# Performance work log

Hardware: AMD Instinct MI355X
Metric: run time of the kernel (lower is better)

Reference implementation:

```python
import jax, jax.numpy as jnp
import numpy as np

D_MODEL = 1024
NUM_HEADS = 16
D_K = D_MODEL // NUM_HEADS
ROPE_THETA = 10000.0


def _rope(x, positions):
    # x: [B, H, S, Dk]; positions: [S] int. Interleaved-pair RoPE, theta=10000.
    half = D_K // 2
    inv_freq = 1.0 / (ROPE_THETA ** (jnp.arange(half, dtype=jnp.float32) * 2.0 / D_K))
    ang = positions.astype(jnp.float32)[:, None] * inv_freq[None, :]  # [S, half]
    cos = jnp.cos(ang)[None, None]  # [1,1,S,half]
    sin = jnp.sin(ang)[None, None]
    x_even = x[..., 0::2]
    x_odd = x[..., 1::2]
    r_even = x_even * cos - x_odd * sin
    r_odd = x_even * sin + x_odd * cos
    out = jnp.stack([r_even, r_odd], axis=-1)  # [B,H,S,half,2]
    return out.reshape(x.shape)


def setup_inputs() -> dict:
    key = jax.random.key(0)
    ks = jax.random.split(key, 5)
    B, S = 4, 2048
    std = (2.0 / (D_MODEL + D_MODEL)) ** 0.5
    return {
        "x": jax.random.normal(ks[0], (B, S, D_MODEL), dtype=jnp.float32),
        "Wq": jax.random.normal(ks[1], (D_MODEL, D_MODEL), dtype=jnp.float32) * std,
        "Wk": jax.random.normal(ks[2], (D_MODEL, D_MODEL), dtype=jnp.float32) * std,
        "Wv": jax.random.normal(ks[3], (D_MODEL, D_MODEL), dtype=jnp.float32) * std,
        "Wo": jax.random.normal(ks[4], (D_MODEL, D_MODEL), dtype=jnp.float32) * std,
        "token_positions": jnp.arange(S, dtype=jnp.int32),
    }


def reference(x, Wq, Wk, Wv, Wo, token_positions):
    B, S, _ = x.shape
    # QKV projections (weights stored [out, in], y = x @ W^T)
    def proj(W):
        y = jnp.einsum('bsi,oi->bso', x, W)
        return y.reshape(B, S, NUM_HEADS, D_K).transpose(0, 2, 1, 3)  # [B,H,S,Dk]
    q = _rope(proj(Wq), token_positions)
    k = _rope(proj(Wk), token_positions)
    v = proj(Wv)
    scores = jnp.einsum('bhqd,bhkd->bhqk', q, k) / jnp.sqrt(jnp.float32(D_K))
    causal = token_positions[:, None] >= token_positions[None, :]  # [S,S]
    scores = jnp.where(causal[None, None], scores, jnp.float32(-1e9))
    probs = jax.nn.softmax(scores, axis=-1)
    attn = jnp.einsum('bhqk,bhkd->bhqd', probs, v)
    attn = attn.transpose(0, 2, 1, 3).reshape(B, S, D_MODEL)
    return jnp.einsum('bsi,oi->bso', attn, Wo)
```

## Files before the change

kernel.cpp:

```cpp
#include <hip/hip_runtime.h>
#include <hip/hip_bf16.h>
#include <math.h>

#define SEQ 2048
#define BATCH 4
#define MROWS (BATCH*SEQ)
#define DMODEL 1024
#define NHEADS 16
#define DKH 64

typedef float f32x4 __attribute__((ext_vector_type(4)));
typedef float f32x16 __attribute__((ext_vector_type(16)));
typedef __bf16 bf16x8 __attribute__((ext_vector_type(8)));
typedef unsigned short u16;
typedef unsigned int u32;
typedef u16 u16x4 __attribute__((ext_vector_type(4)));
typedef u16 u16x8 __attribute__((ext_vector_type(8)));
typedef u32 u32x4v __attribute__((ext_vector_type(4)));

__device__ __forceinline__ u16 f2bf(float f) {
  union { float f; unsigned u; } v; v.f = f;
  unsigned r = v.u + 0x7FFFu + ((v.u >> 16) & 1u);
  return (u16)(r >> 16);
}

__device__ __forceinline__ void async_copy16(const void* g, void* l) {
  __builtin_amdgcn_global_load_lds(
      (const __attribute__((address_space(1))) void*)g,
      (__attribute__((address_space(3))) void*)l, 16, 0, 0);
}

__device__ __forceinline__ u32 cvtpk(float lo, float hi) {
  u32 r;
  asm("v_cvt_pk_bf16_f32 %0, %1, %2" : "=v"(r) : "v"(lo), "v"(hi));
  return r;
}

__global__ __launch_bounds__(256) void k_prep(
    const float* __restrict__ x,
    const float* __restrict__ Wq, const float* __restrict__ Wk,
    const float* __restrict__ Wv, const float* __restrict__ Wo,
    const int* __restrict__ pos,
    u16* __restrict__ xb, u16* __restrict__ Wqb, u16* __restrict__ Wkb,
    u16* __restrict__ Wvb, u16* __restrict__ Wob,
    float* __restrict__ cosT, float* __restrict__ sinT)
{
  const int bid = blockIdx.x, tid = threadIdx.x;
  if (bid < 8192) {
    int i = bid*256 + tid;
    float4 v = ((const float4*)x)[i];
    u16x4 o; o[0]=f2bf(v.x); o[1]=f2bf(v.y); o[2]=f2bf(v.z); o[3]=f2bf(v.w);
    ((u16x4*)xb)[i] = o;
  } else if (bid < 12288) {
    int wi = (bid - 8192) >> 10;
    const float* src = (wi==0)?Wq:(wi==1)?Wk:(wi==2)?Wv:Wo;
    u16* dst = (wi==0)?Wqb:(wi==1)?Wkb:(wi==2)?Wvb:Wob;
    int i = ((bid - 8192) & 1023)*256 + tid;
    float4 v = ((const float4*)src)[i];
    u16x4 o; o[0]=f2bf(v.x); o[1]=f2bf(v.y); o[2]=f2bf(v.z); o[3]=f2bf(v.w);
    ((u16x4*)dst)[i] = o;
  } else {
    int i = (bid - 12288)*256 + tid;
    int s = i >> 5, j = i & 31;
    double p = (double)pos[s];
    double inv = pow(10000.0, -(double)j / 32.0);
    double a = p * inv;
    cosT[i] = (float)cos(a);
    sinT[i] = (float)sin(a);
  }
}

template<int MODE>
__global__ __launch_bounds__(512) void k_gemm2(
    const u16* __restrict__ A,
    const u16* __restrict__ W0, const u16* __restrict__ W1,
    const u16* __restrict__ W2,
    u16* __restrict__ Qo, u16* __restrict__ Ko, u16* __restrict__ Vto,
    float* __restrict__ Fo,
    const float* __restrict__ cosT, const float* __restrict__ sinT)
{
  __shared__ alignas(16) u16 As[3][128*64];
  __shared__ alignas(16) u16 Bs[3][256*64];

  const int B = blockIdx.x;
  const int bm = ((B & 7) << 3) | ((B >> 3) & 7);
  const int y  = B >> 6;
  int proj, bnl;
  const u16* W;
  if constexpr (MODE == 0) {
    proj = y >> 2; bnl = y & 3;
    W = (proj == 0) ? W0 : (proj == 1) ? W1 : W2;
  } else {
    proj = 3; bnl = y; W = W0;
  }

  const int tid = threadIdx.x;
  const int wave = tid >> 6, lane = tid & 63;
  const int lg = lane >> 4, lr = lane & 15;
  const int wm = wave >> 2, wn = wave & 3;

  const u16* Ab = A + (size_t)(bm*128)*DMODEL;
  const u16* Wb = W + (size_t)(bnl*256)*DMODEL;

  f32x4 acc[4][4];
#pragma unroll
  for (int i = 0; i < 4; ++i)
#pragma unroll
    for (int j = 0; j < 4; ++j) acc[i][j] = (f32x4){0,0,0,0};

  auto stage = [&](int buf, int kt) {
    const int k0 = kt * 64;
#pragma unroll
    for (int i = 0; i < 2; ++i) {
      const int idx = i*512 + tid;
      const int row = idx >> 3, ch = idx & 7;
      async_copy16(Ab + (size_t)row*DMODEL + k0 + ((ch ^ (row & 7)) * 8),
                   (char*)As[buf] + idx*16);
    }
#pragma unroll
    for (int i = 0; i < 4; ++i) {
      const int idx = i*512 + tid;
      const int row = idx >> 3, ch = idx & 7;
      async_copy16(Wb + (size_t)row*DMODEL + k0 + ((ch ^ (row & 7)) * 8),
                   (char*)Bs[buf] + idx*16);
    }
  };

  const int NT = DMODEL / 64;
  stage(0, 0);
  stage(1, 1);
  asm volatile("s_waitcnt vmcnt(6)" ::: "memory");
  __builtin_amdgcn_sched_barrier(0);
  __builtin_amdgcn_s_barrier();

  for (int t = 0; t < NT; ++t) {
    const int cur = t % 3;
    if (t + 2 < NT) stage((t + 2) % 3, t + 2);

    const u16* Aw = As[cur];
    const u16* Bw = Bs[cur];
    __builtin_amdgcn_s_setprio(1);
#pragma unroll
    for (int kk = 0; kk < 2; ++kk) {
      bf16x8 bfr[4];
#pragma unroll
      for (int ni = 0; ni < 4; ++ni) {
        const int row = wn*64 + ni*16 + lr;
        bfr[ni] = *(const bf16x8*)&Bw[row*64 + (((kk*4 + lg) ^ (row & 7)) * 8)];
      }
#pragma unroll
      for (int mi = 0; mi < 4; ++mi) {
        const int row = wm*64 + mi*16 + lr;
        bf16x8 af = *(const bf16x8*)&Aw[row*64 + (((kk*4 + lg) ^ (row & 7)) * 8)];
#pragma unroll
        for (int ni = 0; ni < 4; ++ni)
          acc[mi][ni] = __builtin_amdgcn_mfma_f32_16x16x32_bf16(af, bfr[ni], acc[mi][ni], 0, 0, 0);
      }
    }
    __builtin_amdgcn_s_setprio(0);

    if (t + 1 < NT) {
      if (t + 2 < NT) {
        asm volatile("s_waitcnt vmcnt(6)" ::: "memory");
      } else {
        asm volatile("s_waitcnt vmcnt(0)" ::: "memory");
      }
      __builtin_amdgcn_sched_barrier(0);
      __builtin_amdgcn_s_barrier();
    }
  }

#pragma unroll
  for (int mi = 0; mi < 4; ++mi) {
    const int row0 = bm*128 + wm*64 + mi*16 + lg*4;
#pragma unroll
    for (int ni = 0; ni < 4; ++ni) {
      const int col = bnl*256 + wn*64 + ni*16 + lr;
      f32x4 a = acc[mi][ni];
      if constexpr (MODE == 1) {
#pragma unroll
        for (int r = 0; r < 4; ++r) Fo[(size_t)(row0+r)*DMODEL + col] = a[r];
      } else {
        if (proj == 2) {
          const int hh = col >> 6, dd = col & 63;
          const int s0r = row0 & (SEQ-1);
          const int bb = row0 >> 11;
          u16x4 wv;
#pragma unroll
          for (int r = 0; r < 4; ++r) wv[r] = f2bf(a[r]);
          *(u16x4*)&Vto[((size_t)((bb*16+hh)*64 + dd))*SEQ + s0r] = wv;
        } else {
          u16* C = (proj == 0) ? Qo : Ko;
          const float scl = (proj == 0) ? 0.18033688f : 1.0f;
          const int dd = col & 63;
          const int j = dd >> 1;
          const float sgn = (dd & 1) ? 1.0f : -1.0f;
#pragma unroll
          for (int r = 0; r < 4; ++r) {
            const int s = (row0 + r) & (SEQ-1);
            float v = a[r];
            float pv = __shfl_xor(v, 1, 64);
            float c = cosT[s*32 + j], sn = sinT[s*32 + j];
            C[(size_t)(row0+r)*DMODEL + col] = f2bf((v*c + sgn*pv*sn) * scl);
          }
        }
      }
    }
  }
}

__global__ __launch_bounds__(512) void k_attn(
    const u16* __restrict__ Q, const u16* __restrict__ K,
    const u16* __restrict__ Vt, u16* __restrict__ O)
{
  const int B = blockIdx.x;
  const int bh = ((B & 7) << 3) | ((B >> 3) & 7);
  const int qt = 7 - (B >> 6);
  const int b = bh >> 4, h = bh & 15;
  const int wave = threadIdx.x >> 6, lane = threadIdx.x & 63;
  const int ql = lane & 31, hi = lane >> 5, hi4 = hi * 4;
  const int R0 = qt*256 + wave*32;

  __shared__ alignas(16) u16 Ks[2][64*64];
  __shared__ alignas(16) u16 Vs[2][64*64];

  const u16* Qb = Q + (size_t)(b*SEQ)*DMODEL + h*64;
  const u16* Kb = K + (size_t)(b*SEQ)*DMODEL + h*64;
  const u16* Vb = Vt + (size_t)(bh*64)*SEQ;

  bf16x8 qf[4];
#pragma unroll
  for (int j = 0; j < 4; ++j)
    qf[j] = *(const bf16x8*)(Qb + (size_t)(R0 + ql)*DMODEL + j*16 + hi*8);

  union { u16x8 u; bf16x8 v; } onesu;
#pragma unroll
  for (int i = 0; i < 8; ++i) onesu.u[i] = 0x3F80;
  const bf16x8 ones = onesu.v;

  f32x16 o0 = (f32x16)(0.f), o1 = (f32x16)(0.f);
  f32x16 lacc = (f32x16)(0.f);
  float m_run = -INFINITY;
  const float THR2 = 11.5415603f;

  const int KT = (qt + 1) * 4;

  const int qp = (ql & ~12) | ((ql & 4) << 1) | ((ql & 8) >> 1);

  auto stage = [&](int buf, int kt) {
    const int idx = threadIdx.x;
    const int row = idx >> 3, ch = idx & 7;
    const int sch = (ch ^ (row & 7)) * 8;
    const int k0 = kt * 64;
    async_copy16(Kb + (size_t)(k0 + row)*DMODEL + sch, (char*)Ks[buf] + idx*16);
    async_copy16(Vb + (size_t)row*SEQ + k0 + sch,      (char*)Vs[buf] + idx*16);
  };

  stage(0, 0);
  __syncthreads();

  for (int kt = 0; kt < KT; ++kt) {
    const int cur = kt & 1;
    if (kt + 1 < KT) stage(cur ^ 1, kt + 1);

    const int k0 = kt*64;
    if (k0 <= R0 + 31) {
      const u16* Kw = Ks[cur];
      const u16* Vw = Vs[cur];

      bf16x8 ka[2][4];
#pragma unroll
      for (int st = 0; st < 2; ++st)
#pragma unroll
        for (int j = 0; j < 4; ++j) {
          const int rk = st*32 + qp;
          const int c = (2*j + hi) ^ (rk & 7);
          ka[st][j] = *(const bf16x8*)&Kw[rk*64 + c*8];
        }
      f32x16 s0 = (f32x16)(0.f), s1 = (f32x16)(0.f);
#pragma unroll
      for (int j = 0; j < 4; ++j) {
        s0 = __builtin_amdgcn_mfma_f32_32x32x16_bf16(ka[0][j], qf[j], s0, 0, 0, 0);
        s1 = __builtin_amdgcn_mfma_f32_32x32x16_bf16(ka[1][j], qf[j], s1, 0, 0, 0);
      }

      if (k0 + 63 > R0) {
        const int base = k0 - R0;
#pragma unroll
        for (int r = 0; r < 16; ++r) {
          const int kl = (r & 7) + (hi << 3) + ((r & 8) << 1);
          s0[r] = (ql >= base + kl)      ? s0[r] : -1e30f;
          s1[r] = (ql >= base + 32 + kl) ? s1[r] : -1e30f;
        }
      }

      float t[16];
#pragma unroll
      for (int r = 0; r < 16; ++r) t[r] = fmaxf(s0[r], s1[r]);
#pragma unroll
      for (int w = 8; w >= 1; w >>= 1)
#pragma unroll
        for (int r = 0; r < w; ++r) t[r] = fmaxf(t[r], t[r+w]);
      const float mx = fmaxf(t[0], __shfl_xor(t[0], 32, 64));

      if (__any(mx > m_run + THR2)) {
        const float mn = fmaxf(m_run, mx);
        const float al = __builtin_exp2f(m_run - mn);
        m_run = mn;
        lacc[0] *= al;
#pragma unroll
        for (int r = 0; r < 16; ++r) { o0[r] *= al; o1[r] *= al; }
      }

      float e0[16], e1[16];
#pragma unroll
      for (int r = 0; r < 16; ++r) {
        e0[r] = __builtin_exp2f(s0[r] - m_run);
        e1[r] = __builtin_exp2f(s1[r] - m_run);
      }

      bf16x8 pb[4];
#pragma unroll
      for (int sl = 0; sl < 4; ++sl) {
        const float* e = (sl < 2) ? e0 : e1;
        const int o8 = (sl & 1) * 8;
        u32 w0 = cvtpk(e[o8+0], e[o8+1]);
        u32 w1 = cvtpk(e[o8+2], e[o8+3]);
        u32 w2 = cvtpk(e[o8+4], e[o8+5]);
        u32 w3 = cvtpk(e[o8+6], e[o8+7]);
        union { u32x4v u; bf16x8 v; } uu;
        uu.u = (u32x4v){w0, w1, w2, w3};
        pb[sl] = uu.v;
      }

#pragma unroll
      for (int sl = 0; sl < 4; ++sl) {
        const int c0 = 2*sl + hi;
        const int d0 = ql,      ca = (c0 ^ (d0 & 7));
        const int d1 = 32 + ql, cb = (c0 ^ (d1 & 7));
        bf16x8 va0 = *(const bf16x8*)&Vw[d0*64 + ca*8];
        bf16x8 va1 = *(const bf16x8*)&Vw[d1*64 + cb*8];
        o0 = __builtin_amdgcn_mfma_f32_32x32x16_bf16(va0, pb[sl], o0, 0, 0, 0);
        o1 = __builtin_amdgcn_mfma_f32_32x32x16_bf16(va1, pb[sl], o1, 0, 0, 0);
        lacc = __builtin_amdgcn_mfma_f32_32x32x16_bf16(ones, pb[sl], lacc, 0, 0, 0);
      }
    }
    __syncthreads();
  }

  const float inv = 1.0f / lacc[0];
  u16* Orow = O + (size_t)(b*SEQ + R0 + ql)*DMODEL + h*64;
#pragma unroll
  for (int rb = 0; rb < 4; ++rb) {
    u16x4 wA, wB;
#pragma unroll
    for (int j = 0; j < 4; ++j) {
      wA[j] = f2bf(o0[rb*4 + j] * inv);
      wB[j] = f2bf(o1[rb*4 + j] * inv);
    }
    *(u16x4*)(Orow + 8*rb + hi4)      = wA;
    *(u16x4*)(Orow + 32 + 8*rb + hi4) = wB;
  }
}

extern "C" void kernel_launch(void* const* d_in, const int* in_sizes, int n_in,
                              void* d_out, int out_size, void* d_ws, size_t ws_size,
                              hipStream_t stream) {
  const float* x  = (const float*)d_in[0];
  const float* Wq = (const float*)d_in[1];
  const float* Wk = (const float*)d_in[2];
  const float* Wv = (const float*)d_in[3];
  const float* Wo = (const float*)d_in[4];
  const int* pos  = (const int*)d_in[5];
  float* out = (float*)d_out;

  const size_t SZ_X   = (size_t)MROWS*DMODEL*2;
  const size_t SZ_W   = (size_t)DMODEL*DMODEL*2;
  const size_t SZ_TAB = (size_t)SEQ*32*4;
  char* w = (char*)d_ws;
  u16* xb   = (u16*)(w);
  u16* Wqb  = (u16*)(w + SZ_X);
  u16* Wkb  = (u16*)(w + SZ_X + SZ_W);
  u16* Wvb  = (u16*)(w + SZ_X + 2*SZ_W);
  u16* Wob  = (u16*)(w + SZ_X + 3*SZ_W);
  float* cosT = (float*)(w + SZ_X + 4*SZ_W);
  float* sinT = (float*)(w + SZ_X + 4*SZ_W + SZ_TAB);
  u16* Qb   = (u16*)(w + SZ_X + 4*SZ_W + 2*SZ_TAB);
  u16* Kb   = (u16*)(w + 2*SZ_X + 4*SZ_W + 2*SZ_TAB);
  u16* Ob   = (u16*)(w + 3*SZ_X + 4*SZ_W + 2*SZ_TAB);
  u16* Vt   = (u16*)(w + 4*SZ_X + 4*SZ_W + 2*SZ_TAB);
  const size_t need = 5*SZ_X + 4*SZ_W + 2*SZ_TAB;
  if (ws_size < need) return;

  k_prep<<<12544, 256, 0, stream>>>(x, Wq, Wk, Wv, Wo, pos,
                                    xb, Wqb, Wkb, Wvb, Wob, cosT, sinT);
  k_gemm2<0><<<768, 512, 0, stream>>>(
      xb, Wqb, Wkb, Wvb, Qb, Kb, Vt, nullptr, cosT, sinT);
  k_attn<<<512, 512, 0, stream>>>(Qb, Kb, Vt, Ob);
  k_gemm2<1><<<256, 512, 0, stream>>>(
      Ob, Wob, nullptr, nullptr, nullptr, nullptr, nullptr, out, cosT, sinT);
}
```

Measured before the change: 199.3 us.

## Enlarge GEMM tiles to 256x256 with K-step 32 and interleave RoPE table

```diff
diff --git a/kernel.cpp b/kernel.cpp
--- a/kernel.cpp
+++ b/kernel.cpp
@@ -43,7 +43,7 @@
     const int* __restrict__ pos,
     u16* __restrict__ xb, u16* __restrict__ Wqb, u16* __restrict__ Wkb,
     u16* __restrict__ Wvb, u16* __restrict__ Wob,
-    float* __restrict__ cosT, float* __restrict__ sinT)
+    float2* __restrict__ csT)
 {
   const int bid = blockIdx.x, tid = threadIdx.x;
   if (bid < 8192) {
@@ -65,26 +65,27 @@
     double p = (double)pos[s];
     double inv = pow(10000.0, -(double)j / 32.0);
     double a = p * inv;
-    cosT[i] = (float)cos(a);
-    sinT[i] = (float)sin(a);
+    csT[i] = make_float2((float)cos(a), (float)sin(a));
   }
 }
 
 template<int MODE>
-__global__ __launch_bounds__(512) void k_gemm2(
+__global__ __launch_bounds__(512, 2) void k_gemm2(
     const u16* __restrict__ A,
     const u16* __restrict__ W0, const u16* __restrict__ W1,
     const u16* __restrict__ W2,
     u16* __restrict__ Qo, u16* __restrict__ Ko, u16* __restrict__ Vto,
     float* __restrict__ Fo,
-    const float* __restrict__ cosT, const float* __restrict__ sinT)
+    const float2* __restrict__ csT)
 {
-  __shared__ alignas(16) u16 As[3][128*64];
-  __shared__ alignas(16) u16 Bs[3][256*64];
+  __shared__ alignas(16) u16 As[3][256*32];
+  __shared__ alignas(16) u16 Bs[3][256*32];
 
   const int B = blockIdx.x;
-  const int bm = ((B & 7) << 3) | ((B >> 3) & 7);
-  const int y  = B >> 6;
+  const int xcd = B & 7;
+  const int j   = B >> 3;
+  const int bm  = xcd*4 + (j & 3);
+  const int y   = j >> 2;
   int proj, bnl;
   const u16* W;
   if constexpr (MODE == 0) {
@@ -99,37 +100,37 @@
   const int lg = lane >> 4, lr = lane & 15;
   const int wm = wave >> 2, wn = wave & 3;
 
-  const u16* Ab = A + (size_t)(bm*128)*DMODEL;
+  const u16* Ab = A + (size_t)(bm*256)*DMODEL;
   const u16* Wb = W + (size_t)(bnl*256)*DMODEL;
 
-  f32x4 acc[4][4];
-#pragma unroll
-  for (int i = 0; i < 4; ++i)
-#pragma unroll
-    for (int j = 0; j < 4; ++j) acc[i][j] = (f32x4){0,0,0,0};
+  f32x4 acc[8][4];
+#pragma unroll
+  for (int i = 0; i < 8; ++i)
+#pragma unroll
+    for (int jj = 0; jj < 4; ++jj) acc[i][jj] = (f32x4){0,0,0,0};
 
   auto stage = [&](int buf, int kt) {
-    const int k0 = kt * 64;
+    const int k0 = kt * 32;
 #pragma unroll
     for (int i = 0; i < 2; ++i) {
       const int idx = i*512 + tid;
-      const int row = idx >> 3, ch = idx & 7;
-      async_copy16(Ab + (size_t)row*DMODEL + k0 + ((ch ^ (row & 7)) * 8),
+      const int row = idx >> 2, c = idx & 3;
+      async_copy16(Ab + (size_t)row*DMODEL + k0 + ((c ^ ((row >> 1) & 3)) * 8),
                    (char*)As[buf] + idx*16);
     }
 #pragma unroll
-    for (int i = 0; i < 4; ++i) {
+    for (int i = 0; i < 2; ++i) {
       const int idx = i*512 + tid;
-      const int row = idx >> 3, ch = idx & 7;
-      async_copy16(Wb + (size_t)row*DMODEL + k0 + ((ch ^ (row & 7)) * 8),
+      const int row = idx >> 2, c = idx & 3;
+      async_copy16(Wb + (size_t)row*DMODEL + k0 + ((c ^ ((row >> 1) & 3)) * 8),
                    (char*)Bs[buf] + idx*16);
     }
   };
 
-  const int NT = DMODEL / 64;
+  const int NT = DMODEL / 32;
   stage(0, 0);
   stage(1, 1);
-  asm volatile("s_waitcnt vmcnt(6)" ::: "memory");
+  asm volatile("s_waitcnt vmcnt(4)" ::: "memory");
   __builtin_amdgcn_sched_barrier(0);
   __builtin_amdgcn_s_barrier();
 
@@ -139,29 +140,26 @@
 
     const u16* Aw = As[cur];
     const u16* Bw = Bs[cur];
+    bf16x8 bfr[4];
+#pragma unroll
+    for (int ni = 0; ni < 4; ++ni) {
+      const int row = wn*64 + ni*16 + lr;
+      bfr[ni] = *(const bf16x8*)&Bw[row*32 + ((lg ^ ((row >> 1) & 3)) * 8)];
+    }
     __builtin_amdgcn_s_setprio(1);
 #pragma unroll
-    for (int kk = 0; kk < 2; ++kk) {
-      bf16x8 bfr[4];
-#pragma unroll
-      for (int ni = 0; ni < 4; ++ni) {
-        const int row = wn*64 + ni*16 + lr;
-        bfr[ni] = *(const bf16x8*)&Bw[row*64 + (((kk*4 + lg) ^ (row & 7)) * 8)];
-      }
-#pragma unroll
-      for (int mi = 0; mi < 4; ++mi) {
-        const int row = wm*64 + mi*16 + lr;
-        bf16x8 af = *(const bf16x8*)&Aw[row*64 + (((kk*4 + lg) ^ (row & 7)) * 8)];
-#pragma unroll
-        for (int ni = 0; ni < 4; ++ni)
-          acc[mi][ni] = __builtin_amdgcn_mfma_f32_16x16x32_bf16(af, bfr[ni], acc[mi][ni], 0, 0, 0);
-      }
+    for (int mi = 0; mi < 8; ++mi) {
+      const int row = wm*128 + mi*16 + lr;
+      bf16x8 af = *(const bf16x8*)&Aw[row*32 + ((lg ^ ((row >> 1) & 3)) * 8)];
+#pragma unroll
+      for (int ni = 0; ni < 4; ++ni)
+        acc[mi][ni] = __builtin_amdgcn_mfma_f32_16x16x32_bf16(af, bfr[ni], acc[mi][ni], 0, 0, 0);
     }
     __builtin_amdgcn_s_setprio(0);
 
     if (t + 1 < NT) {
       if (t + 2 < NT) {
-        asm volatile("s_waitcnt vmcnt(6)" ::: "memory");
+        asm volatile("s_waitcnt vmcnt(4)" ::: "memory");
       } else {
         asm volatile("s_waitcnt vmcnt(0)" ::: "memory");
       }
@@ -171,8 +169,8 @@
   }
 
 #pragma unroll
-  for (int mi = 0; mi < 4; ++mi) {
-    const int row0 = bm*128 + wm*64 + mi*16 + lg*4;
+  for (int mi = 0; mi < 8; ++mi) {
+    const int row0 = bm*256 + wm*128 + mi*16 + lg*4;
 #pragma unroll
     for (int ni = 0; ni < 4; ++ni) {
       const int col = bnl*256 + wn*64 + ni*16 + lr;
@@ -193,15 +191,15 @@
           u16* C = (proj == 0) ? Qo : Ko;
           const float scl = (proj == 0) ? 0.18033688f : 1.0f;
           const int dd = col & 63;
-          const int j = dd >> 1;
+          const int jj = dd >> 1;
           const float sgn = (dd & 1) ? 1.0f : -1.0f;
 #pragma unroll
           for (int r = 0; r < 4; ++r) {
             const int s = (row0 + r) & (SEQ-1);
             float v = a[r];
             float pv = __shfl_xor(v, 1, 64);
-            float c = cosT[s*32 + j], sn = sinT[s*32 + j];
-            C[(size_t)(row0+r)*DMODEL + col] = f2bf((v*c + sgn*pv*sn) * scl);
+            float2 cs = csT[s*32 + jj];
+            C[(size_t)(row0+r)*DMODEL + col] = f2bf((v*cs.x + sgn*pv*cs.y) * scl);
           }
         }
       }
@@ -244,7 +242,6 @@
   const float THR2 = 11.5415603f;
 
   const int KT = (qt + 1) * 4;
-
   const int qp = (ql & ~12) | ((ql & 4) << 1) | ((ql & 8) >> 1);
 
   auto stage = [&](int buf, int kt) {
@@ -376,27 +373,26 @@
 
   const size_t SZ_X   = (size_t)MROWS*DMODEL*2;
   const size_t SZ_W   = (size_t)DMODEL*DMODEL*2;
-  const size_t SZ_TAB = (size_t)SEQ*32*4;
+  const size_t SZ_TAB = (size_t)SEQ*32*8;
   char* w = (char*)d_ws;
   u16* xb   = (u16*)(w);
   u16* Wqb  = (u16*)(w + SZ_X);
   u16* Wkb  = (u16*)(w + SZ_X + SZ_W);
   u16* Wvb  = (u16*)(w + SZ_X + 2*SZ_W);
   u16* Wob  = (u16*)(w + SZ_X + 3*SZ_W);
-  float* cosT = (float*)(w + SZ_X + 4*SZ_W);
-  float* sinT = (float*)(w + SZ_X + 4*SZ_W + SZ_TAB);
-  u16* Qb   = (u16*)(w + SZ_X + 4*SZ_W + 2*SZ_TAB);
-  u16* Kb   = (u16*)(w + 2*SZ_X + 4*SZ_W + 2*SZ_TAB);
-  u16* Ob   = (u16*)(w + 3*SZ_X + 4*SZ_W + 2*SZ_TAB);
-  u16* Vt   = (u16*)(w + 4*SZ_X + 4*SZ_W + 2*SZ_TAB);
-  const size_t need = 5*SZ_X + 4*SZ_W + 2*SZ_TAB;
+  float2* csT = (float2*)(w + SZ_X + 4*SZ_W);
+  u16* Qb   = (u16*)(w + SZ_X + 4*SZ_W + SZ_TAB);
+  u16* Kb   = (u16*)(w + 2*SZ_X + 4*SZ_W + SZ_TAB);
+  u16* Ob   = (u16*)(w + 3*SZ_X + 4*SZ_W + SZ_TAB);
+  u16* Vt   = (u16*)(w + 4*SZ_X + 4*SZ_W + SZ_TAB);
+  const size_t need = 5*SZ_X + 4*SZ_W + SZ_TAB;
   if (ws_size < need) return;
 
   k_prep<<<12544, 256, 0, stream>>>(x, Wq, Wk, Wv, Wo, pos,
-                                    xb, Wqb, Wkb, Wvb, Wob, cosT, sinT);
-  k_gemm2<0><<<768, 512, 0, stream>>>(
-      xb, Wqb, Wkb, Wvb, Qb, Kb, Vt, nullptr, cosT, sinT);
+                                    xb, Wqb, Wkb, Wvb, Wob, csT);
+  k_gemm2<0><<<384, 512, 0, stream>>>(
+      xb, Wqb, Wkb, Wvb, Qb, Kb, Vt, nullptr, csT);
   k_attn<<<512, 512, 0, stream>>>(Qb, Kb, Vt, Ob);
-  k_gemm2<1><<<256, 512, 0, stream>>>(
-      Ob, Wob, nullptr, nullptr, nullptr, nullptr, nullptr, out, cosT, sinT);
-}
+  k_gemm2<1><<<128, 512, 0, stream>>>(
+      Ob, Wob, nullptr, nullptr, nullptr, nullptr, nullptr, out, csT);
+}
```

Result: slower. 232.5 us (+16.7%).
